# Optimization experiments

Measured on AMD Instinct MI355X. Metric: run time of the kernel, lower is better.

Reference implementation:

```python
import jax, jax.numpy as jnp
import numpy as np

B, T, D = 2, 2048, 1024
H = 16
DH = D // H
SCALE = DH ** -0.5


def setup_inputs() -> dict:
    key = jax.random.key(0)
    ks = jax.random.split(key, 10)
    s = lambda fan_in: 1.0 / np.sqrt(fan_in)
    # weights stored (in, out) so y = x @ W + b (torch Linear transposed)
    return {
        "x": jax.random.normal(ks[0], (B, T, D), dtype=jnp.float32),
        "Wqkv0": jax.random.uniform(ks[1], (D, 3 * D), jnp.float32, -s(D), s(D)),
        "bqkv0": jax.random.uniform(ks[2], (3 * D,), jnp.float32, -s(D), s(D)),
        "Wqkv1": jax.random.uniform(ks[3], (D, 3 * D), jnp.float32, -s(D), s(D)),
        "bqkv1": jax.random.uniform(ks[4], (3 * D,), jnp.float32, -s(D), s(D)),
        "Wg": jax.random.uniform(ks[5], (2 * D, D), jnp.float32, -s(2 * D), s(2 * D)),
        "bg": jax.random.uniform(ks[6], (D,), jnp.float32, -s(2 * D), s(2 * D)),
        "Wo": jax.random.uniform(ks[7], (D, D), jnp.float32, -s(D), s(D)),
        "bo": jax.random.uniform(ks[8], (D,), jnp.float32, -s(D), s(D)),
    }


def _attend(x, Wqkv, bqkv):
    # x: [B,T,D] -> qkv: [B,T,3,H,DH]
    qkv = (x @ Wqkv + bqkv).reshape(B, T, 3, H, DH)
    q, k, v = qkv[:, :, 0], qkv[:, :, 1], qkv[:, :, 2]  # [B,T,H,DH]
    scores = jnp.einsum("bqhd,bkhd->bhqk", q, k) * SCALE
    causal = jnp.tril(jnp.ones((T, T), dtype=bool))
    scores = jnp.where(causal, scores, jnp.finfo(scores.dtype).min)
    attn = jax.nn.softmax(scores, axis=-1)  # dropout is identity in eval mode
    out = jnp.einsum("bhqk,bkhd->bqhd", attn, v)
    return out.reshape(B, T, D)


def reference(x, Wqkv0, bqkv0, Wqkv1, bqkv1, Wg, bg, Wo, bo):
    pred = _attend(x, Wqkv0, bqkv0)
    output = pred
    cumulative = pred
    # n_rounds = 2 -> one correction round
    residual = x - cumulative
    correction = _attend(residual, Wqkv1, bqkv1)
    gate = jax.nn.sigmoid(jnp.concatenate([cumulative, correction], axis=-1) @ Wg + bg)
    gated = gate * correction
    output = output + gated
    return output @ Wo + bo
```

## Files before the change

kernel.cpp:

```cpp
#include <hip/hip_runtime.h>
#include <hip/hip_bf16.h>


typedef __bf16 bf16x8 __attribute__((ext_vector_type(8)));
typedef float f32x4 __attribute__((ext_vector_type(4)));

__device__ __forceinline__ unsigned short f2bf(float f) {
  union { __hip_bfloat16 h; unsigned short u; } cv;
  cv.h = __float2bfloat16(f);
  return cv.u;
}

#define GLD16(gp, lp) __builtin_amdgcn_global_load_lds(                      \
    (const __attribute__((address_space(1))) void*)(gp),                     \
    (__attribute__((address_space(3))) void*)(lp), 16, 0, 0)

__global__ __launch_bounds__(256) void transpose_cast(
    const float* __restrict__ in, __hip_bfloat16* __restrict__ out, int R, int C) {
  __shared__ float t[32][33];
  int bx = blockIdx.x * 32, by = blockIdx.y * 32;
  int tx = threadIdx.x, ty = threadIdx.y;
#pragma unroll
  for (int i = 0; i < 32; i += 8)
    t[ty + i][tx] = in[(size_t)(by + ty + i) * C + bx + tx];
  __syncthreads();
#pragma unroll
  for (int i = 0; i < 32; i += 8)
    out[(size_t)(bx + ty + i) * R + by + tx] = __float2bfloat16(t[tx][ty + i]);
}

__global__ __launch_bounds__(256) void cast_f32_bf16(
    const float* __restrict__ in, __hip_bfloat16* __restrict__ out) {
  size_t e = ((size_t)blockIdx.x * blockDim.x + threadIdx.x) * 4;
  float4 v = *(const float4*)(in + e);
  ushort4 o;
  o.x = f2bf(v.x); o.y = f2bf(v.y); o.z = f2bf(v.z); o.w = f2bf(v.w);
  *(ushort4*)((unsigned short*)out + e) = o;
}

__global__ __launch_bounds__(256) void resid_cast(
    const float* __restrict__ x, const float* __restrict__ pred,
    __hip_bfloat16* __restrict__ catb, __hip_bfloat16* __restrict__ residb) {
  size_t e = ((size_t)blockIdx.x * blockDim.x + threadIdx.x) * 4;
  float4 xv = *(const float4*)(x + e);
  float4 pv = *(const float4*)(pred + e);
  size_t row = e >> 10, col = e & 1023;
  ushort4 pb, rb;
  pb.x = f2bf(pv.x); pb.y = f2bf(pv.y); pb.z = f2bf(pv.z); pb.w = f2bf(pv.w);
  rb.x = f2bf(xv.x - pv.x); rb.y = f2bf(xv.y - pv.y);
  rb.z = f2bf(xv.z - pv.z); rb.w = f2bf(xv.w - pv.w);
  *(ushort4*)((unsigned short*)catb + row * 2048 + col) = pb;
  *(ushort4*)((unsigned short*)residb + e) = rb;
}

__global__ __launch_bounds__(256) void corr_cast(
    const float* __restrict__ corr, __hip_bfloat16* __restrict__ catb) {
  size_t e = ((size_t)blockIdx.x * blockDim.x + threadIdx.x) * 4;
  float4 v = *(const float4*)(corr + e);
  size_t row = e >> 10, col = e & 1023;
  ushort4 o;
  o.x = f2bf(v.x); o.y = f2bf(v.y); o.z = f2bf(v.z); o.w = f2bf(v.w);
  *(ushort4*)((unsigned short*)catb + row * 2048 + 1024 + col) = o;
}

template <int EPI>
__global__ __launch_bounds__(256) void gemm_bf16(
    const __hip_bfloat16* __restrict__ A, const __hip_bfloat16* __restrict__ Bt,
    const float* __restrict__ bias, void* __restrict__ outp,
    const float* __restrict__ aux0, const float* __restrict__ aux1,
    int M, int N, int K) {
  __shared__ __hip_bfloat16 As[128 * 32];
  __shared__ __hip_bfloat16 Bs[128 * 32];
  const int tid = threadIdx.x;
  const int lane = tid & 63, wid = tid >> 6;
  const int wr = wid >> 1, wc = wid & 1;
  const int lr = lane & 15, lk = (lane >> 4) * 8;
  const size_t brow = (size_t)blockIdx.y * 128, bcol = (size_t)blockIdx.x * 128;
  f32x4 acc[4][4] = {};
  for (int k0 = 0; k0 < K; k0 += 32) {
#pragma unroll
    for (int r = 0; r < 2; ++r) {
      int c = tid + r * 256;
      GLD16(A + (brow + (size_t)(c >> 2)) * K + k0 + (c & 3) * 8,
            (__hip_bfloat16*)As + c * 8);
      GLD16(Bt + (bcol + (size_t)(c >> 2)) * K + k0 + (c & 3) * 8,
            (__hip_bfloat16*)Bs + c * 8);
    }
    __syncthreads();
    bf16x8 a[4], b[4];
#pragma unroll
    for (int m = 0; m < 4; ++m)
      a[m] = *(const bf16x8*)(As + (wr * 64 + m * 16 + lr) * 32 + lk);
#pragma unroll
    for (int n = 0; n < 4; ++n)
      b[n] = *(const bf16x8*)(Bs + (wc * 64 + n * 16 + lr) * 32 + lk);
#pragma unroll
    for (int m = 0; m < 4; ++m)
#pragma unroll
      for (int n = 0; n < 4; ++n)
        acc[m][n] = __builtin_amdgcn_mfma_f32_16x16x32_bf16(a[m], b[n], acc[m][n], 0, 0, 0);
    __syncthreads();
  }
  const int r0 = (lane >> 4) * 4, cn = lane & 15;
#pragma unroll
  for (int m = 0; m < 4; ++m)
#pragma unroll
    for (int n = 0; n < 4; ++n) {
      size_t col = bcol + wc * 64 + n * 16 + cn;
      float bv = bias[col];
#pragma unroll
      for (int j = 0; j < 4; ++j) {
        size_t row = brow + wr * 64 + m * 16 + r0 + j;
        float v = acc[m][n][j] + bv;
        if constexpr (EPI == 0) {
          ((__hip_bfloat16*)outp)[row * N + col] = __float2bfloat16(v);
        } else if constexpr (EPI == 1) {
          float g = 1.0f / (1.0f + __expf(-v));
          float val = g * aux0[row * N + col] + aux1[row * N + col];
          ((__hip_bfloat16*)outp)[row * N + col] = __float2bfloat16(val);
        } else {
          ((float*)outp)[row * N + col] = v;
        }
      }
    }
}

__global__ __launch_bounds__(256) void attn_kernel(
    const __hip_bfloat16* __restrict__ qkv, float* __restrict__ outp) {
  const int b = blockIdx.z, h = blockIdx.y, qtp = blockIdx.x;
  const int qlo = qtp, qhi = 31 - qtp;
  const int q0lo = qlo * 64, q0hi = qhi * 64;
  __shared__ __hip_bfloat16 ks[2][64 * 64];
  __shared__ __hip_bfloat16 vts[2][64 * 64];
  __shared__ __hip_bfloat16 qps[8192];
  const int tid = threadIdx.x, lane = tid & 63, w = tid >> 6;
  const int lr = lane & 15, lg = lane >> 4;
  const int sw = lr & 7;
  const size_t rs = 3072;
  const __hip_bfloat16* qbh = qkv + ((size_t)b * 2048 + q0hi) * rs + h * 64;
  const __hip_bfloat16* qbl = qkv + ((size_t)b * 2048 + q0lo) * rs + h * 64;
  const __hip_bfloat16* kb = qkv + (size_t)b * 2048 * rs + 1024 + h * 64;
  const __hip_bfloat16* vb = qkv + (size_t)b * 2048 * rs + 2048 + h * 64;

  float4 vreg[2];
#pragma unroll
  for (int r = 0; r < 2; ++r) {
    int c = tid + r * 256, row = c >> 3, p = c & 7;
    GLD16(qbh + (size_t)row * rs + (p ^ (row & 7)) * 8, qps + c * 8);
    GLD16(qbl + (size_t)row * rs + (p ^ (row & 7)) * 8, qps + 4096 + c * 8);
    GLD16(kb + (size_t)row * rs + (p ^ (row & 7)) * 8, ks[0] + c * 8);
    vreg[r] = *(const float4*)(vb + (size_t)row * rs + p * 8);
  }
  __syncthreads();
  const int qrow = w * 16 + lr;
  const bf16x8 qh0 = *(const bf16x8*)(qps + qrow * 64 + ((lg) ^ (qrow & 7)) * 8);
  const bf16x8 qh1 = *(const bf16x8*)(qps + qrow * 64 + ((4 + lg) ^ (qrow & 7)) * 8);
  const bf16x8 ql0 = *(const bf16x8*)(qps + 4096 + qrow * 64 + ((lg) ^ (qrow & 7)) * 8);
  const bf16x8 ql1 = *(const bf16x8*)(qps + 4096 + qrow * 64 + ((4 + lg) ^ (qrow & 7)) * 8);
#pragma unroll
  for (int r = 0; r < 2; ++r) {
    int c = tid + r * 256, row = c >> 3, seg = c & 7;
    const __hip_bfloat16* e8 = (const __hip_bfloat16*)&vreg[r];
#pragma unroll
    for (int i = 0; i < 8; ++i)
      vts[0][(seg * 8 + i) * 64 + (((row >> 3) ^ i ^ seg)) * 8 + (row & 7)] = e8[i];
  }
  __syncthreads();

  __hip_bfloat16* psh = qps + w * 1024;
  __hip_bfloat16* psl = qps + 4096 + w * 1024;
  float m_hi[4] = {-1e30f, -1e30f, -1e30f, -1e30f}, l_hi[4] = {0, 0, 0, 0};
  float m_lo[4] = {-1e30f, -1e30f, -1e30f, -1e30f}, l_lo[4] = {0, 0, 0, 0};
  f32x4 o_hi[4] = {}, o_lo[4] = {};
  int cur = 0;

  auto process = [&](const bf16x8& qa0, const bf16x8& qa1, bool diag,
                     float* m_run, float* l_run, f32x4* o, __hip_bfloat16* psw) {
    f32x4 s4[4] = {};
#pragma unroll
    for (int n = 0; n < 4; ++n) {
      const int kr = n * 16 + lr;
      bf16x8 k0f = *(const bf16x8*)(ks[cur] + kr * 64 + ((lg) ^ sw) * 8);
      bf16x8 k1f = *(const bf16x8*)(ks[cur] + kr * 64 + ((4 + lg) ^ sw) * 8);
      s4[n] = __builtin_amdgcn_mfma_f32_16x16x32_bf16(qa0, k0f, s4[n], 0, 0, 0);
      s4[n] = __builtin_amdgcn_mfma_f32_16x16x32_bf16(qa1, k1f, s4[n], 0, 0, 0);
    }
    float p[4][4], mloc[4];
#pragma unroll
    for (int j = 0; j < 4; ++j) {
      float mm = -1e30f;
#pragma unroll
      for (int n = 0; n < 4; ++n) {
        float v = s4[n][j] * 0.125f;
        if (diag && (n * 16 + lr) > (w * 16 + lg * 4 + j)) v = -1e30f;
        p[n][j] = v;
        mm = fmaxf(mm, v);
      }
      mloc[j] = mm;
    }
#pragma unroll
    for (int off = 1; off < 16; off <<= 1)
#pragma unroll
      for (int j = 0; j < 4; ++j)
        mloc[j] = fmaxf(mloc[j], __shfl_xor(mloc[j], off, 16));
    float sc[4], ls[4];
#pragma unroll
    for (int j = 0; j < 4; ++j) {
      float mn = fmaxf(m_run[j], mloc[j]);
      sc[j] = __expf(m_run[j] - mn);
      m_run[j] = mn;
      float s = 0.f;
#pragma unroll
      for (int n = 0; n < 4; ++n) { p[n][j] = __expf(p[n][j] - mn); s += p[n][j]; }
      ls[j] = s;
    }
#pragma unroll
    for (int off = 1; off < 16; off <<= 1)
#pragma unroll
      for (int j = 0; j < 4; ++j) ls[j] += __shfl_xor(ls[j], off, 16);
#pragma unroll
    for (int j = 0; j < 4; ++j) l_run[j] = l_run[j] * sc[j] + ls[j];
#pragma unroll
    for (int n = 0; n < 4; ++n)
#pragma unroll
      for (int j = 0; j < 4; ++j) o[n][j] *= sc[j];
#pragma unroll
    for (int n = 0; n < 4; ++n)
#pragma unroll
      for (int j = 0; j < 4; ++j) {
        const int prow = lg * 4 + j;
        const int phys = (n * 2 + (lr >> 3)) ^ (prow & 7);
        psw[prow * 64 + phys * 8 + (lr & 7)] = __float2bfloat16(p[n][j]);
      }
    bf16x8 pa0 = *(const bf16x8*)(&psw[lr * 64 + ((lg) ^ sw) * 8]);
    bf16x8 pa1 = *(const bf16x8*)(&psw[lr * 64 + ((4 + lg) ^ sw) * 8]);
#pragma unroll
    for (int n = 0; n < 4; ++n) {
      const int vdh = n * 16 + lr;
      const int swv = (vdh & 7) ^ ((vdh >> 3) & 7);
      bf16x8 v0f = *(const bf16x8*)(vts[cur] + vdh * 64 + ((lg) ^ swv) * 8);
      bf16x8 v1f = *(const bf16x8*)(vts[cur] + vdh * 64 + ((4 + lg) ^ swv) * 8);
      o[n] = __builtin_amdgcn_mfma_f32_16x16x32_bf16(pa0, v0f, o[n], 0, 0, 0);
      o[n] = __builtin_amdgcn_mfma_f32_16x16x32_bf16(pa1, v1f, o[n], 0, 0, 0);
    }
  };

  for (int kvt = 0; kvt <= qhi; ++kvt) {
    const int nxt = cur ^ 1;
    const bool pf = (kvt < qhi);
    if (pf) {
      const int kv1 = (kvt + 1) * 64;
#pragma unroll
      for (int r = 0; r < 2; ++r) {
        int c = tid + r * 256, row = c >> 3, p = c & 7;
        GLD16(kb + (size_t)(kv1 + row) * rs + (p ^ (row & 7)) * 8, ks[nxt] + c * 8);
        vreg[r] = *(const float4*)(vb + (size_t)(kv1 + row) * rs + p * 8);
      }
    }
    process(qh0, qh1, kvt == qhi, m_hi, l_hi, o_hi, psh);
    if (kvt <= qlo) process(ql0, ql1, kvt == qlo, m_lo, l_lo, o_lo, psl);
    if (pf) {
#pragma unroll
      for (int r = 0; r < 2; ++r) {
        int c = tid + r * 256, row = c >> 3, seg = c & 7;
        const __hip_bfloat16* e8 = (const __hip_bfloat16*)&vreg[r];
#pragma unroll
        for (int i = 0; i < 8; ++i)
          vts[nxt][(seg * 8 + i) * 64 + (((row >> 3) ^ i ^ seg)) * 8 + (row & 7)] = e8[i];
      }
    }
    __syncthreads();
    cur = nxt;
  }
#pragma unroll
  for (int j = 0; j < 4; ++j) {
    float invh = 1.0f / l_hi[j], invl = 1.0f / l_lo[j];
    size_t rowh = (size_t)b * 2048 + q0hi + w * 16 + lg * 4 + j;
    size_t rowl = (size_t)b * 2048 + q0lo + w * 16 + lg * 4 + j;
#pragma unroll
    for (int n = 0; n < 4; ++n) {
      outp[rowh * 1024 + h * 64 + n * 16 + lr] = o_hi[n][j] * invh;
      outp[rowl * 1024 + h * 64 + n * 16 + lr] = o_lo[n][j] * invl;
    }
  }
}

extern "C" void kernel_launch(void* const* d_in, const int* in_sizes, int n_in,
                              void* d_out, int out_size, void* d_ws, size_t ws_size,
                              hipStream_t stream) {
  const float* x     = (const float*)d_in[0];
  const float* Wqkv0 = (const float*)d_in[1];
  const float* bqkv0 = (const float*)d_in[2];
  const float* Wqkv1 = (const float*)d_in[3];
  const float* bqkv1 = (const float*)d_in[4];
  const float* Wg    = (const float*)d_in[5];
  const float* bg    = (const float*)d_in[6];
  const float* Wo    = (const float*)d_in[7];
  const float* bo    = (const float*)d_in[8];
  float* out = (float*)d_out;

  char* ws = (char*)d_ws;
  __hip_bfloat16* xb   = (__hip_bfloat16*)(ws);
  __hip_bfloat16* qkv  = (__hip_bfloat16*)(ws + 8388608);
  float*          pred = (float*)(ws + 33554432);
  float*          corr = (float*)(ws + 50331648);
  __hip_bfloat16* catb = (__hip_bfloat16*)(ws + 67108864);
  __hip_bfloat16* Wt0  = (__hip_bfloat16*)(ws + 83886080);
  __hip_bfloat16* Wt1  = (__hip_bfloat16*)(ws + 90177536);
  __hip_bfloat16* Wgt  = (__hip_bfloat16*)(ws + 96468992);
  __hip_bfloat16* Wot  = (__hip_bfloat16*)(ws + 100663296);

  dim3 tb(32, 8);
  transpose_cast<<<dim3(3072 / 32, 1024 / 32), tb, 0, stream>>>(Wqkv0, Wt0, 1024, 3072);
  transpose_cast<<<dim3(3072 / 32, 1024 / 32), tb, 0, stream>>>(Wqkv1, Wt1, 1024, 3072);
  transpose_cast<<<dim3(1024 / 32, 2048 / 32), tb, 0, stream>>>(Wg, Wgt, 2048, 1024);
  transpose_cast<<<dim3(1024 / 32, 1024 / 32), tb, 0, stream>>>(Wo, Wot, 1024, 1024);
  cast_f32_bf16<<<4096, 256, 0, stream>>>(x, xb);

  gemm_bf16<0><<<dim3(24, 32), 256, 0, stream>>>(xb, Wt0, bqkv0, (void*)qkv,
                                                 nullptr, nullptr, 4096, 3072, 1024);
  attn_kernel<<<dim3(16, 16, 2), 256, 0, stream>>>(qkv, pred);
  resid_cast<<<4096, 256, 0, stream>>>(x, pred, catb, xb);
  gemm_bf16<0><<<dim3(24, 32), 256, 0, stream>>>(xb, Wt1, bqkv1, (void*)qkv,
                                                 nullptr, nullptr, 4096, 3072, 1024);
  attn_kernel<<<dim3(16, 16, 2), 256, 0, stream>>>(qkv, corr);
  corr_cast<<<4096, 256, 0, stream>>>(corr, catb);
  gemm_bf16<1><<<dim3(8, 32), 256, 0, stream>>>(catb, Wgt, bg, (void*)xb,
                                                corr, pred, 4096, 1024, 2048);
  gemm_bf16<2><<<dim3(8, 32), 256, 0, stream>>>(xb, Wot, bo, (void*)out,
                                                nullptr, nullptr, 4096, 1024, 1024);
}
```

Baseline: 352.9 us.

## Split hi/lo query tiles across separate waves in 512-thread attention blocks

The attention kernel now launches 512 threads per block. Waves 0-3 process the high query tile and waves 4-7 process the low tile, where before each wave handled both tiles serially. Each thread loads one chunk of K/V per iteration instead of two. This doubles wave-level parallelism and cuts per-thread register state. In exchange, the low-tile waves sit idle at barriers after their diagonal while the hi waves finish, and the register budget per thread is tighter.

Measured after the change: 428.9 us. 21.5% more time.

```diff
diff --git a/kernel.cpp b/kernel.cpp
--- a/kernel.cpp
+++ b/kernel.cpp
@@ -125,7 +125,7 @@
     }
 }
 
-__global__ __launch_bounds__(256) void attn_kernel(
+__global__ __launch_bounds__(512) void attn_kernel(
     const __hip_bfloat16* __restrict__ qkv, float* __restrict__ outp) {
   const int b = blockIdx.z, h = blockIdx.y, qtp = blockIdx.x;
   const int qlo = qtp, qhi = 31 - qtp;
@@ -134,6 +134,8 @@
   __shared__ __hip_bfloat16 vts[2][64 * 64];
   __shared__ __hip_bfloat16 qps[8192];
   const int tid = threadIdx.x, lane = tid & 63, w = tid >> 6;
+  const bool is_hi = (w < 4);
+  const int wrow = (w & 3) * 16;
   const int lr = lane & 15, lg = lane >> 4;
   const int sw = lr & 7;
   const size_t rs = 3072;
@@ -142,146 +144,131 @@
   const __hip_bfloat16* kb = qkv + (size_t)b * 2048 * rs + 1024 + h * 64;
   const __hip_bfloat16* vb = qkv + (size_t)b * 2048 * rs + 2048 + h * 64;
 
-  float4 vreg[2];
-#pragma unroll
-  for (int r = 0; r < 2; ++r) {
-    int c = tid + r * 256, row = c >> 3, p = c & 7;
+  float4 vreg;
+  {
+    int c = tid, row = c >> 3, p = c & 7;
     GLD16(qbh + (size_t)row * rs + (p ^ (row & 7)) * 8, qps + c * 8);
     GLD16(qbl + (size_t)row * rs + (p ^ (row & 7)) * 8, qps + 4096 + c * 8);
     GLD16(kb + (size_t)row * rs + (p ^ (row & 7)) * 8, ks[0] + c * 8);
-    vreg[r] = *(const float4*)(vb + (size_t)row * rs + p * 8);
+    vreg = *(const float4*)(vb + (size_t)row * rs + p * 8);
   }
   __syncthreads();
-  const int qrow = w * 16 + lr;
-  const bf16x8 qh0 = *(const bf16x8*)(qps + qrow * 64 + ((lg) ^ (qrow & 7)) * 8);
-  const bf16x8 qh1 = *(const bf16x8*)(qps + qrow * 64 + ((4 + lg) ^ (qrow & 7)) * 8);
-  const bf16x8 ql0 = *(const bf16x8*)(qps + 4096 + qrow * 64 + ((lg) ^ (qrow & 7)) * 8);
-  const bf16x8 ql1 = *(const bf16x8*)(qps + 4096 + qrow * 64 + ((4 + lg) ^ (qrow & 7)) * 8);
-#pragma unroll
-  for (int r = 0; r < 2; ++r) {
-    int c = tid + r * 256, row = c >> 3, seg = c & 7;
-    const __hip_bfloat16* e8 = (const __hip_bfloat16*)&vreg[r];
+  const int qrow = wrow + lr;
+  const __hip_bfloat16* qsrc = qps + (is_hi ? 0 : 4096);
+  const bf16x8 qa0 = *(const bf16x8*)(qsrc + qrow * 64 + ((lg) ^ (qrow & 7)) * 8);
+  const bf16x8 qa1 = *(const bf16x8*)(qsrc + qrow * 64 + ((4 + lg) ^ (qrow & 7)) * 8);
+  {
+    int c = tid, row = c >> 3, seg = c & 7;
+    const __hip_bfloat16* e8 = (const __hip_bfloat16*)&vreg;
 #pragma unroll
     for (int i = 0; i < 8; ++i)
       vts[0][(seg * 8 + i) * 64 + (((row >> 3) ^ i ^ seg)) * 8 + (row & 7)] = e8[i];
   }
   __syncthreads();
 
-  __hip_bfloat16* psh = qps + w * 1024;
-  __hip_bfloat16* psl = qps + 4096 + w * 1024;
-  float m_hi[4] = {-1e30f, -1e30f, -1e30f, -1e30f}, l_hi[4] = {0, 0, 0, 0};
-  float m_lo[4] = {-1e30f, -1e30f, -1e30f, -1e30f}, l_lo[4] = {0, 0, 0, 0};
-  f32x4 o_hi[4] = {}, o_lo[4] = {};
+  __hip_bfloat16* psw = qps + w * 1024;
+  float m_run[4] = {-1e30f, -1e30f, -1e30f, -1e30f}, l_run[4] = {0, 0, 0, 0};
+  f32x4 o[4] = {};
   int cur = 0;
-
-  auto process = [&](const bf16x8& qa0, const bf16x8& qa1, bool diag,
-                     float* m_run, float* l_run, f32x4* o, __hip_bfloat16* psw) {
-    f32x4 s4[4] = {};
-#pragma unroll
-    for (int n = 0; n < 4; ++n) {
-      const int kr = n * 16 + lr;
-      bf16x8 k0f = *(const bf16x8*)(ks[cur] + kr * 64 + ((lg) ^ sw) * 8);
-      bf16x8 k1f = *(const bf16x8*)(ks[cur] + kr * 64 + ((4 + lg) ^ sw) * 8);
-      s4[n] = __builtin_amdgcn_mfma_f32_16x16x32_bf16(qa0, k0f, s4[n], 0, 0, 0);
-      s4[n] = __builtin_amdgcn_mfma_f32_16x16x32_bf16(qa1, k1f, s4[n], 0, 0, 0);
-    }
-    float p[4][4], mloc[4];
-#pragma unroll
-    for (int j = 0; j < 4; ++j) {
-      float mm = -1e30f;
-#pragma unroll
-      for (int n = 0; n < 4; ++n) {
-        float v = s4[n][j] * 0.125f;
-        if (diag && (n * 16 + lr) > (w * 16 + lg * 4 + j)) v = -1e30f;
-        p[n][j] = v;
-        mm = fmaxf(mm, v);
-      }
-      mloc[j] = mm;
-    }
-#pragma unroll
-    for (int off = 1; off < 16; off <<= 1)
-#pragma unroll
-      for (int j = 0; j < 4; ++j)
-        mloc[j] = fmaxf(mloc[j], __shfl_xor(mloc[j], off, 16));
-    float sc[4], ls[4];
-#pragma unroll
-    for (int j = 0; j < 4; ++j) {
-      float mn = fmaxf(m_run[j], mloc[j]);
-      sc[j] = __expf(m_run[j] - mn);
-      m_run[j] = mn;
-      float s = 0.f;
-#pragma unroll
-      for (int n = 0; n < 4; ++n) { p[n][j] = __expf(p[n][j] - mn); s += p[n][j]; }
-      ls[j] = s;
-    }
-#pragma unroll
-    for (int off = 1; off < 16; off <<= 1)
-#pragma unroll
-      for (int j = 0; j < 4; ++j) ls[j] += __shfl_xor(ls[j], off, 16);
-#pragma unroll
-    for (int j = 0; j < 4; ++j) l_run[j] = l_run[j] * sc[j] + ls[j];
-#pragma unroll
-    for (int n = 0; n < 4; ++n)
-#pragma unroll
-      for (int j = 0; j < 4; ++j) o[n][j] *= sc[j];
-#pragma unroll
-    for (int n = 0; n < 4; ++n)
-#pragma unroll
-      for (int j = 0; j < 4; ++j) {
-        const int prow = lg * 4 + j;
-        const int phys = (n * 2 + (lr >> 3)) ^ (prow & 7);
-        psw[prow * 64 + phys * 8 + (lr & 7)] = __float2bfloat16(p[n][j]);
-      }
-    bf16x8 pa0 = *(const bf16x8*)(&psw[lr * 64 + ((lg) ^ sw) * 8]);
-    bf16x8 pa1 = *(const bf16x8*)(&psw[lr * 64 + ((4 + lg) ^ sw) * 8]);
-#pragma unroll
-    for (int n = 0; n < 4; ++n) {
-      const int vdh = n * 16 + lr;
-      const int swv = (vdh & 7) ^ ((vdh >> 3) & 7);
-      bf16x8 v0f = *(const bf16x8*)(vts[cur] + vdh * 64 + ((lg) ^ swv) * 8);
-      bf16x8 v1f = *(const bf16x8*)(vts[cur] + vdh * 64 + ((4 + lg) ^ swv) * 8);
-      o[n] = __builtin_amdgcn_mfma_f32_16x16x32_bf16(pa0, v0f, o[n], 0, 0, 0);
-      o[n] = __builtin_amdgcn_mfma_f32_16x16x32_bf16(pa1, v1f, o[n], 0, 0, 0);
-    }
-  };
+  const int mydiag = is_hi ? qhi : qlo;
 
   for (int kvt = 0; kvt <= qhi; ++kvt) {
     const int nxt = cur ^ 1;
     const bool pf = (kvt < qhi);
     if (pf) {
       const int kv1 = (kvt + 1) * 64;
-#pragma unroll
-      for (int r = 0; r < 2; ++r) {
-        int c = tid + r * 256, row = c >> 3, p = c & 7;
-        GLD16(kb + (size_t)(kv1 + row) * rs + (p ^ (row & 7)) * 8, ks[nxt] + c * 8);
-        vreg[r] = *(const float4*)(vb + (size_t)(kv1 + row) * rs + p * 8);
-      }
-    }
-    process(qh0, qh1, kvt == qhi, m_hi, l_hi, o_hi, psh);
-    if (kvt <= qlo) process(ql0, ql1, kvt == qlo, m_lo, l_lo, o_lo, psl);
+      int c = tid, row = c >> 3, p = c & 7;
+      GLD16(kb + (size_t)(kv1 + row) * rs + (p ^ (row & 7)) * 8, ks[nxt] + c * 8);
+      vreg = *(const float4*)(vb + (size_t)(kv1 + row) * rs + p * 8);
+    }
+    if (kvt <= mydiag) {
+      const bool diag = (kvt == mydiag);
+      f32x4 s4[4] = {};
+#pragma unroll
+      for (int n = 0; n < 4; ++n) {
+        const int kr = n * 16 + lr;
+        bf16x8 k0f = *(const bf16x8*)(ks[cur] + kr * 64 + ((lg) ^ sw) * 8);
+        bf16x8 k1f = *(const bf16x8*)(ks[cur] + kr * 64 + ((4 + lg) ^ sw) * 8);
+        s4[n] = __builtin_amdgcn_mfma_f32_16x16x32_bf16(qa0, k0f, s4[n], 0, 0, 0);
+        s4[n] = __builtin_amdgcn_mfma_f32_16x16x32_bf16(qa1, k1f, s4[n], 0, 0, 0);
+      }
+      float p[4][4], mloc[4];
+#pragma unroll
+      for (int j = 0; j < 4; ++j) {
+        float mm = -1e30f;
+#pragma unroll
+        for (int n = 0; n < 4; ++n) {
+          float v = s4[n][j] * 0.125f;
+          if (diag && (n * 16 + lr) > (wrow + lg * 4 + j)) v = -1e30f;
+          p[n][j] = v;
+          mm = fmaxf(mm, v);
+        }
+        mloc[j] = mm;
+      }
+#pragma unroll
+      for (int off = 1; off < 16; off <<= 1)
+#pragma unroll
+        for (int j = 0; j < 4; ++j)
+          mloc[j] = fmaxf(mloc[j], __shfl_xor(mloc[j], off, 16));
+      float sc[4], ls[4];
+#pragma unroll
+      for (int j = 0; j < 4; ++j) {
+        float mn = fmaxf(m_run[j], mloc[j]);
+        sc[j] = __expf(m_run[j] - mn);
+        m_run[j] = mn;
+        float s = 0.f;
+#pragma unroll
+        for (int n = 0; n < 4; ++n) { p[n][j] = __expf(p[n][j] - mn); s += p[n][j]; }
+        ls[j] = s;
+      }
+#pragma unroll
+      for (int off = 1; off < 16; off <<= 1)
+#pragma unroll
+        for (int j = 0; j < 4; ++j) ls[j] += __shfl_xor(ls[j], off, 16);
+#pragma unroll
+      for (int j = 0; j < 4; ++j) l_run[j] = l_run[j] * sc[j] + ls[j];
+#pragma unroll
+      for (int n = 0; n < 4; ++n)
+#pragma unroll
+        for (int j = 0; j < 4; ++j) o[n][j] *= sc[j];
+#pragma unroll
+      for (int n = 0; n < 4; ++n)
+#pragma unroll
+        for (int j = 0; j < 4; ++j) {
+          const int prow = lg * 4 + j;
+          const int phys = (n * 2 + (lr >> 3)) ^ (prow & 7);
+          psw[prow * 64 + phys * 8 + (lr & 7)] = __float2bfloat16(p[n][j]);
+        }
+      bf16x8 pa0 = *(const bf16x8*)(&psw[lr * 64 + ((lg) ^ sw) * 8]);
+      bf16x8 pa1 = *(const bf16x8*)(&psw[lr * 64 + ((4 + lg) ^ sw) * 8]);
+#pragma unroll
+      for (int n = 0; n < 4; ++n) {
+        const int vdh = n * 16 + lr;
+        const int swv = (vdh & 7) ^ ((vdh >> 3) & 7);
+        bf16x8 v0f = *(const bf16x8*)(vts[cur] + vdh * 64 + ((lg) ^ swv) * 8);
+        bf16x8 v1f = *(const bf16x8*)(vts[cur] + vdh * 64 + ((4 + lg) ^ swv) * 8);
+        o[n] = __builtin_amdgcn_mfma_f32_16x16x32_bf16(pa0, v0f, o[n], 0, 0, 0);
+        o[n] = __builtin_amdgcn_mfma_f32_16x16x32_bf16(pa1, v1f, o[n], 0, 0, 0);
+      }
+    }
     if (pf) {
-#pragma unroll
-      for (int r = 0; r < 2; ++r) {
-        int c = tid + r * 256, row = c >> 3, seg = c & 7;
-        const __hip_bfloat16* e8 = (const __hip_bfloat16*)&vreg[r];
-#pragma unroll
-        for (int i = 0; i < 8; ++i)
-          vts[nxt][(seg * 8 + i) * 64 + (((row >> 3) ^ i ^ seg)) * 8 + (row & 7)] = e8[i];
-      }
+      int c = tid, row = c >> 3, seg = c & 7;
+      const __hip_bfloat16* e8 = (const __hip_bfloat16*)&vreg;
+#pragma unroll
+      for (int i = 0; i < 8; ++i)
+        vts[nxt][(seg * 8 + i) * 64 + (((row >> 3) ^ i ^ seg)) * 8 + (row & 7)] = e8[i];
     }
     __syncthreads();
     cur = nxt;
   }
+  const int q0 = is_hi ? q0hi : q0lo;
 #pragma unroll
   for (int j = 0; j < 4; ++j) {
-    float invh = 1.0f / l_hi[j], invl = 1.0f / l_lo[j];
-    size_t rowh = (size_t)b * 2048 + q0hi + w * 16 + lg * 4 + j;
-    size_t rowl = (size_t)b * 2048 + q0lo + w * 16 + lg * 4 + j;
-#pragma unroll
-    for (int n = 0; n < 4; ++n) {
-      outp[rowh * 1024 + h * 64 + n * 16 + lr] = o_hi[n][j] * invh;
-      outp[rowl * 1024 + h * 64 + n * 16 + lr] = o_lo[n][j] * invl;
-    }
+    float inv = 1.0f / l_run[j];
+    size_t row = (size_t)b * 2048 + q0 + wrow + lg * 4 + j;
+#pragma unroll
+    for (int n = 0; n < 4; ++n)
+      outp[row * 1024 + h * 64 + n * 16 + lr] = o[n][j] * inv;
   }
 }
 
@@ -319,11 +306,11 @@
 
   gemm_bf16<0><<<dim3(24, 32), 256, 0, stream>>>(xb, Wt0, bqkv0, (void*)qkv,
                                                  nullptr, nullptr, 4096, 3072, 1024);
-  attn_kernel<<<dim3(16, 16, 2), 256, 0, stream>>>(qkv, pred);
+  attn_kernel<<<dim3(16, 16, 2), 512, 0, stream>>>(qkv, pred);
   resid_cast<<<4096, 256, 0, stream>>>(x, pred, catb, xb);
   gemm_bf16<0><<<dim3(24, 32), 256, 0, stream>>>(xb, Wt1, bqkv1, (void*)qkv,
                                                  nullptr, nullptr, 4096, 3072, 1024);
-  attn_kernel<<<dim3(16, 16, 2), 256, 0, stream>>>(qkv, corr);
+  attn_kernel<<<dim3(16, 16, 2), 512, 0, stream>>>(qkv, corr);
   corr_cast<<<4096, 256, 0, stream>>>(corr, catb);
   gemm_bf16<1><<<dim3(8, 32), 256, 0, stream>>>(catb, Wgt, bg, (void*)xb,
                                                 corr, pred, 4096, 1024, 2048);
```

## Double-buffer GEMM LDS tiles and interleave hi/lo attention tile processing

Applied to the files above, without the earlier changes.

The bf16 GEMM now keeps two LDS buffers for A and B, so the next K slice is loaded while MFMAs run on the current one. This removes one barrier per iteration and hides global-load latency, at the cost of doubling GEMM shared memory. The attention loop inlines the process lambda and interleaves the high and low query tiles: the K fragments are loaded once for both QK^T MFMA chains, and the V fragments once for both PV chains. This is meant to reuse LDS reads and give the scheduler more independent MFMA work, but it raises register pressure.

After: 354.1 us. No clear change (+0.4%).

```diff
diff --git a/kernel.cpp b/kernel.cpp
--- a/kernel.cpp
+++ b/kernel.cpp
@@ -69,37 +69,48 @@
     const float* __restrict__ bias, void* __restrict__ outp,
     const float* __restrict__ aux0, const float* __restrict__ aux1,
     int M, int N, int K) {
-  __shared__ __hip_bfloat16 As[128 * 32];
-  __shared__ __hip_bfloat16 Bs[128 * 32];
+  __shared__ __hip_bfloat16 As[2][128 * 32];
+  __shared__ __hip_bfloat16 Bs[2][128 * 32];
   const int tid = threadIdx.x;
   const int lane = tid & 63, wid = tid >> 6;
   const int wr = wid >> 1, wc = wid & 1;
   const int lr = lane & 15, lk = (lane >> 4) * 8;
   const size_t brow = (size_t)blockIdx.y * 128, bcol = (size_t)blockIdx.x * 128;
   f32x4 acc[4][4] = {};
+#pragma unroll
+  for (int r = 0; r < 2; ++r) {
+    int c = tid + r * 256;
+    GLD16(A + (brow + (size_t)(c >> 2)) * K + (c & 3) * 8, As[0] + c * 8);
+    GLD16(Bt + (bcol + (size_t)(c >> 2)) * K + (c & 3) * 8, Bs[0] + c * 8);
+  }
+  __syncthreads();
+  int cur = 0;
   for (int k0 = 0; k0 < K; k0 += 32) {
-#pragma unroll
-    for (int r = 0; r < 2; ++r) {
-      int c = tid + r * 256;
-      GLD16(A + (brow + (size_t)(c >> 2)) * K + k0 + (c & 3) * 8,
-            (__hip_bfloat16*)As + c * 8);
-      GLD16(Bt + (bcol + (size_t)(c >> 2)) * K + k0 + (c & 3) * 8,
-            (__hip_bfloat16*)Bs + c * 8);
-    }
-    __syncthreads();
+    const int nxt = cur ^ 1;
+    if (k0 + 32 < K) {
+#pragma unroll
+      for (int r = 0; r < 2; ++r) {
+        int c = tid + r * 256;
+        GLD16(A + (brow + (size_t)(c >> 2)) * K + k0 + 32 + (c & 3) * 8,
+              As[nxt] + c * 8);
+        GLD16(Bt + (bcol + (size_t)(c >> 2)) * K + k0 + 32 + (c & 3) * 8,
+              Bs[nxt] + c * 8);
+      }
+    }
     bf16x8 a[4], b[4];
 #pragma unroll
     for (int m = 0; m < 4; ++m)
-      a[m] = *(const bf16x8*)(As + (wr * 64 + m * 16 + lr) * 32 + lk);
+      a[m] = *(const bf16x8*)(As[cur] + (wr * 64 + m * 16 + lr) * 32 + lk);
 #pragma unroll
     for (int n = 0; n < 4; ++n)
-      b[n] = *(const bf16x8*)(Bs + (wc * 64 + n * 16 + lr) * 32 + lk);
+      b[n] = *(const bf16x8*)(Bs[cur] + (wc * 64 + n * 16 + lr) * 32 + lk);
 #pragma unroll
     for (int m = 0; m < 4; ++m)
 #pragma unroll
       for (int n = 0; n < 4; ++n)
         acc[m][n] = __builtin_amdgcn_mfma_f32_16x16x32_bf16(a[m], b[n], acc[m][n], 0, 0, 0);
     __syncthreads();
+    cur = nxt;
   }
   const int r0 = (lane >> 4) * 4, cn = lane & 15;
 #pragma unroll
@@ -174,91 +185,150 @@
   f32x4 o_hi[4] = {}, o_lo[4] = {};
   int cur = 0;
 
-  auto process = [&](const bf16x8& qa0, const bf16x8& qa1, bool diag,
-                     float* m_run, float* l_run, f32x4* o, __hip_bfloat16* psw) {
-    f32x4 s4[4] = {};
+  for (int kvt = 0; kvt <= qhi; ++kvt) {
+    const int nxt = cur ^ 1;
+    const bool pf = (kvt < qhi);
+    const bool lo_act = (kvt <= qlo);
+    if (pf) {
+      const int kv1 = (kvt + 1) * 64;
+#pragma unroll
+      for (int r = 0; r < 2; ++r) {
+        int c = tid + r * 256, row = c >> 3, p = c & 7;
+        GLD16(kb + (size_t)(kv1 + row) * rs + (p ^ (row & 7)) * 8, ks[nxt] + c * 8);
+        vreg[r] = *(const float4*)(vb + (size_t)(kv1 + row) * rs + p * 8);
+      }
+    }
+    f32x4 sh[4] = {}, sl[4] = {};
 #pragma unroll
     for (int n = 0; n < 4; ++n) {
       const int kr = n * 16 + lr;
       bf16x8 k0f = *(const bf16x8*)(ks[cur] + kr * 64 + ((lg) ^ sw) * 8);
       bf16x8 k1f = *(const bf16x8*)(ks[cur] + kr * 64 + ((4 + lg) ^ sw) * 8);
-      s4[n] = __builtin_amdgcn_mfma_f32_16x16x32_bf16(qa0, k0f, s4[n], 0, 0, 0);
-      s4[n] = __builtin_amdgcn_mfma_f32_16x16x32_bf16(qa1, k1f, s4[n], 0, 0, 0);
-    }
-    float p[4][4], mloc[4];
-#pragma unroll
-    for (int j = 0; j < 4; ++j) {
-      float mm = -1e30f;
-#pragma unroll
-      for (int n = 0; n < 4; ++n) {
-        float v = s4[n][j] * 0.125f;
-        if (diag && (n * 16 + lr) > (w * 16 + lg * 4 + j)) v = -1e30f;
-        p[n][j] = v;
-        mm = fmaxf(mm, v);
-      }
-      mloc[j] = mm;
-    }
-#pragma unroll
-    for (int off = 1; off < 16; off <<= 1)
-#pragma unroll
-      for (int j = 0; j < 4; ++j)
-        mloc[j] = fmaxf(mloc[j], __shfl_xor(mloc[j], off, 16));
-    float sc[4], ls[4];
-#pragma unroll
-    for (int j = 0; j < 4; ++j) {
-      float mn = fmaxf(m_run[j], mloc[j]);
-      sc[j] = __expf(m_run[j] - mn);
-      m_run[j] = mn;
-      float s = 0.f;
-#pragma unroll
-      for (int n = 0; n < 4; ++n) { p[n][j] = __expf(p[n][j] - mn); s += p[n][j]; }
-      ls[j] = s;
-    }
-#pragma unroll
-    for (int off = 1; off < 16; off <<= 1)
-#pragma unroll
-      for (int j = 0; j < 4; ++j) ls[j] += __shfl_xor(ls[j], off, 16);
-#pragma unroll
-    for (int j = 0; j < 4; ++j) l_run[j] = l_run[j] * sc[j] + ls[j];
-#pragma unroll
-    for (int n = 0; n < 4; ++n)
-#pragma unroll
-      for (int j = 0; j < 4; ++j) o[n][j] *= sc[j];
-#pragma unroll
-    for (int n = 0; n < 4; ++n)
+      sh[n] = __builtin_amdgcn_mfma_f32_16x16x32_bf16(qh0, k0f, sh[n], 0, 0, 0);
+      sh[n] = __builtin_amdgcn_mfma_f32_16x16x32_bf16(qh1, k1f, sh[n], 0, 0, 0);
+      if (lo_act) {
+        sl[n] = __builtin_amdgcn_mfma_f32_16x16x32_bf16(ql0, k0f, sl[n], 0, 0, 0);
+        sl[n] = __builtin_amdgcn_mfma_f32_16x16x32_bf16(ql1, k1f, sl[n], 0, 0, 0);
+      }
+    }
+    bf16x8 pa_h0, pa_h1, pa_l0, pa_l1;
+    {
+      const bool diag = (kvt == qhi);
+      float p[4][4], mloc[4];
 #pragma unroll
       for (int j = 0; j < 4; ++j) {
-        const int prow = lg * 4 + j;
-        const int phys = (n * 2 + (lr >> 3)) ^ (prow & 7);
-        psw[prow * 64 + phys * 8 + (lr & 7)] = __float2bfloat16(p[n][j]);
-      }
-    bf16x8 pa0 = *(const bf16x8*)(&psw[lr * 64 + ((lg) ^ sw) * 8]);
-    bf16x8 pa1 = *(const bf16x8*)(&psw[lr * 64 + ((4 + lg) ^ sw) * 8]);
+        float mm = -1e30f;
+#pragma unroll
+        for (int n = 0; n < 4; ++n) {
+          float v = sh[n][j] * 0.125f;
+          if (diag && (n * 16 + lr) > (w * 16 + lg * 4 + j)) v = -1e30f;
+          p[n][j] = v;
+          mm = fmaxf(mm, v);
+        }
+        mloc[j] = mm;
+      }
+#pragma unroll
+      for (int off = 1; off < 16; off <<= 1)
+#pragma unroll
+        for (int j = 0; j < 4; ++j)
+          mloc[j] = fmaxf(mloc[j], __shfl_xor(mloc[j], off, 16));
+      float sc[4], ls[4];
+#pragma unroll
+      for (int j = 0; j < 4; ++j) {
+        float mn = fmaxf(m_hi[j], mloc[j]);
+        sc[j] = __expf(m_hi[j] - mn);
+        m_hi[j] = mn;
+        float s = 0.f;
+#pragma unroll
+        for (int n = 0; n < 4; ++n) { p[n][j] = __expf(p[n][j] - mn); s += p[n][j]; }
+        ls[j] = s;
+      }
+#pragma unroll
+      for (int off = 1; off < 16; off <<= 1)
+#pragma unroll
+        for (int j = 0; j < 4; ++j) ls[j] += __shfl_xor(ls[j], off, 16);
+#pragma unroll
+      for (int j = 0; j < 4; ++j) l_hi[j] = l_hi[j] * sc[j] + ls[j];
+#pragma unroll
+      for (int n = 0; n < 4; ++n)
+#pragma unroll
+        for (int j = 0; j < 4; ++j) o_hi[n][j] *= sc[j];
+#pragma unroll
+      for (int n = 0; n < 4; ++n)
+#pragma unroll
+        for (int j = 0; j < 4; ++j) {
+          const int prow = lg * 4 + j;
+          const int phys = (n * 2 + (lr >> 3)) ^ (prow & 7);
+          psh[prow * 64 + phys * 8 + (lr & 7)] = __float2bfloat16(p[n][j]);
+        }
+      pa_h0 = *(const bf16x8*)(&psh[lr * 64 + ((lg) ^ sw) * 8]);
+      pa_h1 = *(const bf16x8*)(&psh[lr * 64 + ((4 + lg) ^ sw) * 8]);
+    }
+    if (lo_act) {
+      const bool diag = (kvt == qlo);
+      float p[4][4], mloc[4];
+#pragma unroll
+      for (int j = 0; j < 4; ++j) {
+        float mm = -1e30f;
+#pragma unroll
+        for (int n = 0; n < 4; ++n) {
+          float v = sl[n][j] * 0.125f;
+          if (diag && (n * 16 + lr) > (w * 16 + lg * 4 + j)) v = -1e30f;
+          p[n][j] = v;
+          mm = fmaxf(mm, v);
+        }
+        mloc[j] = mm;
+      }
+#pragma unroll
+      for (int off = 1; off < 16; off <<= 1)
+#pragma unroll
+        for (int j = 0; j < 4; ++j)
+          mloc[j] = fmaxf(mloc[j], __shfl_xor(mloc[j], off, 16));
+      float sc[4], ls[4];
+#pragma unroll
+      for (int j = 0; j < 4; ++j) {
+        float mn = fmaxf(m_lo[j], mloc[j]);
+        sc[j] = __expf(m_lo[j] - mn);
+        m_lo[j] = mn;
+        float s = 0.f;
+#pragma unroll
+        for (int n = 0; n < 4; ++n) { p[n][j] = __expf(p[n][j] - mn); s += p[n][j]; }
+        ls[j] = s;
+      }
+#pragma unroll
+      for (int off = 1; off < 16; off <<= 1)
+#pragma unroll
+        for (int j = 0; j < 4; ++j) ls[j] += __shfl_xor(ls[j], off, 16);
+#pragma unroll
+      for (int j = 0; j < 4; ++j) l_lo[j] = l_lo[j] * sc[j] + ls[j];
+#pragma unroll
+      for (int n = 0; n < 4; ++n)
+#pragma unroll
+        for (int j = 0; j < 4; ++j) o_lo[n][j] *= sc[j];
+#pragma unroll
+      for (int n = 0; n < 4; ++n)
+#pragma unroll
+        for (int j = 0; j < 4; ++j) {
+          const int prow = lg * 4 + j;
+          const int phys = (n * 2 + (lr >> 3)) ^ (prow & 7);
+          psl[prow * 64 + phys * 8 + (lr & 7)] = __float2bfloat16(p[n][j]);
+        }
+      pa_l0 = *(const bf16x8*)(&psl[lr * 64 + ((lg) ^ sw) * 8]);
+      pa_l1 = *(const bf16x8*)(&psl[lr * 64 + ((4 + lg) ^ sw) * 8]);
+    }
 #pragma unroll
     for (int n = 0; n < 4; ++n) {
       const int vdh = n * 16 + lr;
       const int swv = (vdh & 7) ^ ((vdh >> 3) & 7);
       bf16x8 v0f = *(const bf16x8*)(vts[cur] + vdh * 64 + ((lg) ^ swv) * 8);
       bf16x8 v1f = *(const bf16x8*)(vts[cur] + vdh * 64 + ((4 + lg) ^ swv) * 8);
-      o[n] = __builtin_amdgcn_mfma_f32_16x16x32_bf16(pa0, v0f, o[n], 0, 0, 0);
-      o[n] = __builtin_amdgcn_mfma_f32_16x16x32_bf16(pa1, v1f, o[n], 0, 0, 0);
-    }
-  };
-
-  for (int kvt = 0; kvt <= qhi; ++kvt) {
-    const int nxt = cur ^ 1;
-    const bool pf = (kvt < qhi);
-    if (pf) {
-      const int kv1 = (kvt + 1) * 64;
-#pragma unroll
-      for (int r = 0; r < 2; ++r) {
-        int c = tid + r * 256, row = c >> 3, p = c & 7;
-        GLD16(kb + (size_t)(kv1 + row) * rs + (p ^ (row & 7)) * 8, ks[nxt] + c * 8);
-        vreg[r] = *(const float4*)(vb + (size_t)(kv1 + row) * rs + p * 8);
-      }
-    }
-    process(qh0, qh1, kvt == qhi, m_hi, l_hi, o_hi, psh);
-    if (kvt <= qlo) process(ql0, ql1, kvt == qlo, m_lo, l_lo, o_lo, psl);
+      o_hi[n] = __builtin_amdgcn_mfma_f32_16x16x32_bf16(pa_h0, v0f, o_hi[n], 0, 0, 0);
+      o_hi[n] = __builtin_amdgcn_mfma_f32_16x16x32_bf16(pa_h1, v1f, o_hi[n], 0, 0, 0);
+      if (lo_act) {
+        o_lo[n] = __builtin_amdgcn_mfma_f32_16x16x32_bf16(pa_l0, v0f, o_lo[n], 0, 0, 0);
+        o_lo[n] = __builtin_amdgcn_mfma_f32_16x16x32_bf16(pa_l1, v1f, o_lo[n], 0, 0, 0);
+      }
+    }
     if (pf) {
 #pragma unroll
       for (int r = 0; r < 2; ++r) {
```

## Double-buffer GEMM LDS loads and transpose S tile for per-lane softmax stats

Applied to the files above, without the earlier changes.

The GEMM kernel now double-buffers its A/B LDS tiles, issuing the next k-slice's global-to-LDS loads before computing the current one, so one barrier per iteration is removed and load latency overlaps MFMA work. The attention kernel swaps MFMA operands so each lane holds one query row's scores. The row max and sum then become scalars per lane, reduced with two cross-group shuffles instead of a 16-lane butterfly over four values. The rescale factors and final normalisation are broadcast back to the O-accumulator layout with shuffles, and the P tile store is rewritten for the new layout. This adds LDS use in the GEMM and relies on the global_load_lds writes to the next buffer being complete by the next barrier.

Result: faster. 309.3 us (-12.3%).

```diff
diff --git a/kernel.cpp b/kernel.cpp
--- a/kernel.cpp
+++ b/kernel.cpp
@@ -69,37 +69,48 @@
     const float* __restrict__ bias, void* __restrict__ outp,
     const float* __restrict__ aux0, const float* __restrict__ aux1,
     int M, int N, int K) {
-  __shared__ __hip_bfloat16 As[128 * 32];
-  __shared__ __hip_bfloat16 Bs[128 * 32];
+  __shared__ __hip_bfloat16 As[2][128 * 32];
+  __shared__ __hip_bfloat16 Bs[2][128 * 32];
   const int tid = threadIdx.x;
   const int lane = tid & 63, wid = tid >> 6;
   const int wr = wid >> 1, wc = wid & 1;
   const int lr = lane & 15, lk = (lane >> 4) * 8;
   const size_t brow = (size_t)blockIdx.y * 128, bcol = (size_t)blockIdx.x * 128;
   f32x4 acc[4][4] = {};
+#pragma unroll
+  for (int r = 0; r < 2; ++r) {
+    int c = tid + r * 256;
+    GLD16(A + (brow + (size_t)(c >> 2)) * K + (c & 3) * 8, As[0] + c * 8);
+    GLD16(Bt + (bcol + (size_t)(c >> 2)) * K + (c & 3) * 8, Bs[0] + c * 8);
+  }
+  __syncthreads();
+  int cur = 0;
   for (int k0 = 0; k0 < K; k0 += 32) {
-#pragma unroll
-    for (int r = 0; r < 2; ++r) {
-      int c = tid + r * 256;
-      GLD16(A + (brow + (size_t)(c >> 2)) * K + k0 + (c & 3) * 8,
-            (__hip_bfloat16*)As + c * 8);
-      GLD16(Bt + (bcol + (size_t)(c >> 2)) * K + k0 + (c & 3) * 8,
-            (__hip_bfloat16*)Bs + c * 8);
-    }
-    __syncthreads();
+    const int nxt = cur ^ 1;
+    if (k0 + 32 < K) {
+#pragma unroll
+      for (int r = 0; r < 2; ++r) {
+        int c = tid + r * 256;
+        GLD16(A + (brow + (size_t)(c >> 2)) * K + k0 + 32 + (c & 3) * 8,
+              As[nxt] + c * 8);
+        GLD16(Bt + (bcol + (size_t)(c >> 2)) * K + k0 + 32 + (c & 3) * 8,
+              Bs[nxt] + c * 8);
+      }
+    }
     bf16x8 a[4], b[4];
 #pragma unroll
     for (int m = 0; m < 4; ++m)
-      a[m] = *(const bf16x8*)(As + (wr * 64 + m * 16 + lr) * 32 + lk);
-#pragma unroll
-    for (int n = 0; n < 4; ++n)
-      b[n] = *(const bf16x8*)(Bs + (wc * 64 + n * 16 + lr) * 32 + lk);
+      a[m] = *(const bf16x8*)(As[cur] + (wr * 64 + m * 16 + lr) * 32 + lk);
+#pragma unroll
+    for (int n = 0; n < 4; ++n)
+      b[n] = *(const bf16x8*)(Bs[cur] + (wc * 64 + n * 16 + lr) * 32 + lk);
 #pragma unroll
     for (int m = 0; m < 4; ++m)
 #pragma unroll
       for (int n = 0; n < 4; ++n)
         acc[m][n] = __builtin_amdgcn_mfma_f32_16x16x32_bf16(a[m], b[n], acc[m][n], 0, 0, 0);
     __syncthreads();
+    cur = nxt;
   }
   const int r0 = (lane >> 4) * 4, cn = lane & 15;
 #pragma unroll
@@ -169,69 +180,58 @@
 
   __hip_bfloat16* psh = qps + w * 1024;
   __hip_bfloat16* psl = qps + 4096 + w * 1024;
-  float m_hi[4] = {-1e30f, -1e30f, -1e30f, -1e30f}, l_hi[4] = {0, 0, 0, 0};
-  float m_lo[4] = {-1e30f, -1e30f, -1e30f, -1e30f}, l_lo[4] = {0, 0, 0, 0};
+  float m_hi = -1e30f, l_hi = 0.f, m_lo = -1e30f, l_lo = 0.f;
   f32x4 o_hi[4] = {}, o_lo[4] = {};
   int cur = 0;
 
   auto process = [&](const bf16x8& qa0, const bf16x8& qa1, bool diag,
-                     float* m_run, float* l_run, f32x4* o, __hip_bfloat16* psw) {
+                     float& m_run, float& l_run, f32x4* o, __hip_bfloat16* psw) {
     f32x4 s4[4] = {};
 #pragma unroll
     for (int n = 0; n < 4; ++n) {
       const int kr = n * 16 + lr;
       bf16x8 k0f = *(const bf16x8*)(ks[cur] + kr * 64 + ((lg) ^ sw) * 8);
       bf16x8 k1f = *(const bf16x8*)(ks[cur] + kr * 64 + ((4 + lg) ^ sw) * 8);
-      s4[n] = __builtin_amdgcn_mfma_f32_16x16x32_bf16(qa0, k0f, s4[n], 0, 0, 0);
-      s4[n] = __builtin_amdgcn_mfma_f32_16x16x32_bf16(qa1, k1f, s4[n], 0, 0, 0);
-    }
-    float p[4][4], mloc[4];
-#pragma unroll
-    for (int j = 0; j < 4; ++j) {
-      float mm = -1e30f;
-#pragma unroll
-      for (int n = 0; n < 4; ++n) {
+      s4[n] = __builtin_amdgcn_mfma_f32_16x16x32_bf16(k0f, qa0, s4[n], 0, 0, 0);
+      s4[n] = __builtin_amdgcn_mfma_f32_16x16x32_bf16(k1f, qa1, s4[n], 0, 0, 0);
+    }
+    float p[4][4];
+    float mloc = -1e30f;
+#pragma unroll
+    for (int n = 0; n < 4; ++n)
+#pragma unroll
+      for (int j = 0; j < 4; ++j) {
         float v = s4[n][j] * 0.125f;
-        if (diag && (n * 16 + lr) > (w * 16 + lg * 4 + j)) v = -1e30f;
+        if (diag && (n * 16 + lg * 4 + j) > (w * 16 + lr)) v = -1e30f;
         p[n][j] = v;
-        mm = fmaxf(mm, v);
-      }
-      mloc[j] = mm;
-    }
-#pragma unroll
-    for (int off = 1; off < 16; off <<= 1)
+        mloc = fmaxf(mloc, v);
+      }
+    mloc = fmaxf(mloc, __shfl_xor(mloc, 16));
+    mloc = fmaxf(mloc, __shfl_xor(mloc, 32));
+    const float mn = fmaxf(m_run, mloc);
+    const float sc = __expf(m_run - mn);
+    m_run = mn;
+    float ls = 0.f;
+#pragma unroll
+    for (int n = 0; n < 4; ++n)
+#pragma unroll
+      for (int j = 0; j < 4; ++j) { p[n][j] = __expf(p[n][j] - mn); ls += p[n][j]; }
+    ls += __shfl_xor(ls, 16);
+    ls += __shfl_xor(ls, 32);
+    l_run = l_run * sc + ls;
+    float scb[4];
+#pragma unroll
+    for (int j = 0; j < 4; ++j) scb[j] = __shfl(sc, lg * 4 + j);
+#pragma unroll
+    for (int n = 0; n < 4; ++n)
+#pragma unroll
+      for (int j = 0; j < 4; ++j) o[n][j] *= scb[j];
+#pragma unroll
+    for (int n = 0; n < 4; ++n)
 #pragma unroll
       for (int j = 0; j < 4; ++j)
-        mloc[j] = fmaxf(mloc[j], __shfl_xor(mloc[j], off, 16));
-    float sc[4], ls[4];
-#pragma unroll
-    for (int j = 0; j < 4; ++j) {
-      float mn = fmaxf(m_run[j], mloc[j]);
-      sc[j] = __expf(m_run[j] - mn);
-      m_run[j] = mn;
-      float s = 0.f;
-#pragma unroll
-      for (int n = 0; n < 4; ++n) { p[n][j] = __expf(p[n][j] - mn); s += p[n][j]; }
-      ls[j] = s;
-    }
-#pragma unroll
-    for (int off = 1; off < 16; off <<= 1)
-#pragma unroll
-      for (int j = 0; j < 4; ++j) ls[j] += __shfl_xor(ls[j], off, 16);
-#pragma unroll
-    for (int j = 0; j < 4; ++j) l_run[j] = l_run[j] * sc[j] + ls[j];
-#pragma unroll
-    for (int n = 0; n < 4; ++n)
-#pragma unroll
-      for (int j = 0; j < 4; ++j) o[n][j] *= sc[j];
-#pragma unroll
-    for (int n = 0; n < 4; ++n)
-#pragma unroll
-      for (int j = 0; j < 4; ++j) {
-        const int prow = lg * 4 + j;
-        const int phys = (n * 2 + (lr >> 3)) ^ (prow & 7);
-        psw[prow * 64 + phys * 8 + (lr & 7)] = __float2bfloat16(p[n][j]);
-      }
+        psw[lr * 64 + ((n * 2 + (lg >> 1)) ^ sw) * 8 + (lg & 1) * 4 + j] =
+            __float2bfloat16(p[n][j]);
     bf16x8 pa0 = *(const bf16x8*)(&psw[lr * 64 + ((lg) ^ sw) * 8]);
     bf16x8 pa1 = *(const bf16x8*)(&psw[lr * 64 + ((4 + lg) ^ sw) * 8]);
 #pragma unroll
@@ -272,15 +272,17 @@
     __syncthreads();
     cur = nxt;
   }
+  const float linv_h = 1.0f / l_hi, linv_l = 1.0f / l_lo;
 #pragma unroll
   for (int j = 0; j < 4; ++j) {
-    float invh = 1.0f / l_hi[j], invl = 1.0f / l_lo[j];
+    const float lih = __shfl(linv_h, lg * 4 + j);
+    const float lil = __shfl(linv_l, lg * 4 + j);
     size_t rowh = (size_t)b * 2048 + q0hi + w * 16 + lg * 4 + j;
     size_t rowl = (size_t)b * 2048 + q0lo + w * 16 + lg * 4 + j;
 #pragma unroll
     for (int n = 0; n < 4; ++n) {
-      outp[rowh * 1024 + h * 64 + n * 16 + lr] = o_hi[n][j] * invh;
-      outp[rowl * 1024 + h * 64 + n * 16 + lr] = o_lo[n][j] * invl;
+      outp[rowh * 1024 + h * 64 + n * 16 + lr] = o_hi[n][j] * lih;
+      outp[rowl * 1024 + h * 64 + n * 16 + lr] = o_lo[n][j] * lil;
     }
   }
 }
```
